# Kernel tuning notes

Measured on AMD Instinct MI355X. Metric: run time of the kernel, lower is better.

## Reference

```python
import jax, jax.numpy as jnp
import numpy as np

G, K, H = 4, 8, 512  # gate_dim, k blocks, block size

def setup_inputs() -> dict:
    key = jax.random.key(0)
    kx, kA, kB = jax.random.split(key, 3)
    x = jax.random.normal(kx, (4096, K * H), dtype=jnp.float32)
    # xavier_normal for (h,h) matrices: std = sqrt(2/(h+h)) = 1/sqrt(h)
    std = 1.0 / np.sqrt(H)
    A = jax.random.normal(kA, (G, H, H), dtype=jnp.float32) * std
    B = jax.random.normal(kB, (G, H, H), dtype=jnp.float32) * std
    return {"x": x, "A": A, "B": B}

def reference(x, A, B):
    # W = blockdiag-style: row block (g,i), col block j -> A_g if i==j else B_g.
    # y[b, g, i, :] = x_i @ A_g^T + (sum_j x_j - x_i) @ B_g^T
    #              = x_i @ (A_g - B_g)^T + S @ B_g^T
    bsz = x.shape[0]
    x3 = x.reshape(bsz, K, H)                      # [B, k, h]
    S = x3.sum(axis=1)                              # [B, h]
    diag_part = jnp.einsum('bkh,gph->bgkp', x3, A - B)   # [B, g, k, h]
    sum_part = jnp.einsum('bh,gph->bgp', S, B)           # [B, g, h]
    out = diag_part + sum_part[:, :, None, :]
    return out.reshape(bsz, G * K * H)
```

## Files before the change

kernel.cpp:

```cpp
#include <hip/hip_runtime.h>

typedef _Float16 f16x8 __attribute__((ext_vector_type(8)));
typedef _Float16 f16x4 __attribute__((ext_vector_type(4)));
typedef _Float16 f16x2 __attribute__((ext_vector_type(2)));
typedef float f32x4 __attribute__((ext_vector_type(4)));
typedef float f32x2 __attribute__((ext_vector_type(2)));

#define GLD_LDS16(gp, lp)                                                        \
  __builtin_amdgcn_global_load_lds(                                              \
      (const __attribute__((address_space(1))) void*)(gp),                       \
      (__attribute__((address_space(3))) void*)(lp), 16, 0, 0)

__global__ void prep_weights_k(const float* __restrict__ A, const float* __restrict__ B,
                               _Float16* __restrict__ Cw, _Float16* __restrict__ Bw) {
  int gid = blockIdx.x * 256 + threadIdx.x;
  f32x4 a = ((const f32x4*)A)[gid];
  f32x4 b = ((const f32x4*)B)[gid];
  f16x4 c, bb;
  c.x = (_Float16)(a.x - b.x); c.y = (_Float16)(a.y - b.y);
  c.z = (_Float16)(a.z - b.z); c.w = (_Float16)(a.w - b.w);
  bb.x = (_Float16)b.x; bb.y = (_Float16)b.y;
  bb.z = (_Float16)b.z; bb.w = (_Float16)b.w;
  ((f16x4*)Cw)[gid] = c;
  ((f16x4*)Bw)[gid] = bb;
}

__global__ void prep_x_k(const float* __restrict__ x, _Float16* __restrict__ xh,
                         _Float16* __restrict__ Sh) {
  int b = blockIdx.x, t = threadIdx.x;
  const f32x2* xr = (const f32x2*)(x + (size_t)b * 4096);
  f16x2* xo = (f16x2*)xh + (size_t)b * 2048;
  float s0 = 0.f, s1 = 0.f;
#pragma unroll
  for (int i = 0; i < 8; ++i) {
    f32x2 v = xr[i * 256 + t];
    f16x2 h;
    h.x = (_Float16)v.x; h.y = (_Float16)v.y;
    xo[i * 256 + t] = h;
    s0 += v.x; s1 += v.y;
  }
  f16x2 sv;
  sv.x = (_Float16)s0; sv.y = (_Float16)s1;
  ((f16x2*)Sh)[(size_t)b * 256 + t] = sv;
}

__global__ __launch_bounds__(256) void gemm_fused_k(const _Float16* __restrict__ Am,
                                                    const _Float16* __restrict__ Cw,
                                                    const _Float16* __restrict__ Bw,
                                                    const _Float16* __restrict__ Sh,
                                                    float* __restrict__ out) {
  __shared__ __align__(16) _Float16 lA[128 * 32];
  __shared__ __align__(16) _Float16 lW[128 * 32];
  __shared__ __align__(16) _Float16 lV[128 * 32];
  __shared__ __align__(16) _Float16 lS[16 * 32];

  const int tid = threadIdx.x;
  const int lane = tid & 63;
  const int wv = tid >> 6;
  const int tile_n = blockIdx.x & 15;
  const int tile_m = blockIdx.x >> 4;

  const _Float16* gA[2];
  const _Float16* gW[2];
  const _Float16* gV[2];
  _Float16* lpA[2];
  _Float16* lpW[2];
  _Float16* lpV[2];
#pragma unroll
  for (int i = 0; i < 2; ++i) {
    int c = i * 256 + tid;
    int row = c >> 2;
    int lc = (c & 3) ^ ((row >> 1) & 3);
    gA[i] = Am + ((size_t)(tile_m * 128 + row) * 512 + lc * 8);
    gW[i] = Cw + ((size_t)(tile_n * 128 + row) * 512 + lc * 8);
    gV[i] = Bw + ((size_t)(tile_n * 128 + row) * 512 + lc * 8);
    lpA[i] = &lA[(i * 256 + wv * 64) * 8];
    lpW[i] = &lW[(i * 256 + wv * 64) * 8];
    lpV[i] = &lV[(i * 256 + wv * 64) * 8];
  }
  const _Float16* gS =
      Sh + ((size_t)(tile_m * 16 + (lane >> 2)) * 512 + (lane & 3) * 8);

  const int lm = lane & 15;
  const int q = lane >> 4;
  const int mw = (wv >> 1) * 64;
  const int nw = (wv & 1) * 64;

  int aoff[4], boff[4], voff[2];
#pragma unroll
  for (int f = 0; f < 4; ++f) {
    int rA = mw + f * 16 + lm;
    aoff[f] = rA * 32 + (q ^ ((rA >> 1) & 3)) * 8;
    int rB = nw + f * 16 + lm;
    boff[f] = rB * 32 + (q ^ ((rB >> 1) & 3)) * 8;
  }
#pragma unroll
  for (int f = 0; f < 2; ++f) {
    int rV = wv * 32 + f * 16 + lm;
    voff[f] = rV * 32 + (q ^ ((rV >> 1) & 3)) * 8;
  }
  const int soff = lm * 32 + q * 8;

  f32x4 acc[4][4];
  f32x4 tacc[2];
#pragma unroll
  for (int im = 0; im < 4; ++im)
#pragma unroll
    for (int in = 0; in < 4; ++in) acc[im][in] = (f32x4){0.f, 0.f, 0.f, 0.f};
#pragma unroll
  for (int f = 0; f < 2; ++f) tacc[f] = (f32x4){0.f, 0.f, 0.f, 0.f};

  for (int kt = 0; kt < 16; ++kt) {
    __syncthreads();
#pragma unroll
    for (int i = 0; i < 2; ++i) {
      GLD_LDS16(gA[i] + kt * 32, lpA[i]);
      GLD_LDS16(gW[i] + kt * 32, lpW[i]);
      GLD_LDS16(gV[i] + kt * 32, lpV[i]);
    }
    if (wv == 0) GLD_LDS16(gS + kt * 32, &lS[0]);
    __syncthreads();
    f16x8 af[4], bf[4], vf[2], sf;
    sf = *(const f16x8*)&lS[soff];
#pragma unroll
    for (int f = 0; f < 4; ++f) {
      af[f] = *(const f16x8*)&lA[aoff[f]];
      bf[f] = *(const f16x8*)&lW[boff[f]];
    }
#pragma unroll
    for (int f = 0; f < 2; ++f) vf[f] = *(const f16x8*)&lV[voff[f]];
#pragma unroll
    for (int im = 0; im < 4; ++im)
#pragma unroll
      for (int in = 0; in < 4; ++in)
        acc[im][in] =
            __builtin_amdgcn_mfma_f32_16x16x32_f16(af[im], bf[in], acc[im][in], 0, 0, 0);
#pragma unroll
    for (int f = 0; f < 2; ++f)
      tacc[f] = __builtin_amdgcn_mfma_f32_16x16x32_f16(sf, vf[f], tacc[f], 0, 0, 0);
  }

  __syncthreads();
  float* lT = (float*)lA;
#pragma unroll
  for (int f = 0; f < 2; ++f) {
    int colb = wv * 32 + f * 16 + lm;
#pragma unroll
    for (int r = 0; r < 4; ++r) lT[(q * 4 + r) * 128 + colb] = tacc[f][r];
  }
  __syncthreads();

#pragma unroll
  for (int im = 0; im < 4; ++im) {
    const int mloc = mw + im * 16 + q * 4;
    const int mbase = tile_m * 128 + mloc;
    const int b = mbase >> 3;
    const int bl = mloc >> 3;
#pragma unroll
    for (int in = 0; in < 4; ++in) {
      const int cl = nw + in * 16 + lm;
      const int col = tile_n * 128 + cl;
      const float tv = lT[bl * 128 + cl];
      f32x4 v = acc[im][in];
      float* op = out + (size_t)b * 16384 + (size_t)(col >> 9) * 4096 +
                  (size_t)(mbase & 7) * 512 + (col & 511);
#pragma unroll
      for (int r = 0; r < 4; ++r) op[r * 512] = v[r] + tv;
    }
  }
}

extern "C" void kernel_launch(void* const* d_in, const int* in_sizes, int n_in,
                              void* d_out, int out_size, void* d_ws, size_t ws_size,
                              hipStream_t stream) {
  const float* x = (const float*)d_in[0];
  const float* A = (const float*)d_in[1];
  const float* B = (const float*)d_in[2];
  float* out = (float*)d_out;
  char* ws = (char*)d_ws;

  _Float16* xh = (_Float16*)(ws);
  _Float16* Sh = (_Float16*)(ws + 33554432u);
  _Float16* Cw = (_Float16*)(ws + 37748736u);
  _Float16* Bw = (_Float16*)(ws + 39845888u);

  prep_weights_k<<<1024, 256, 0, stream>>>(A, B, Cw, Bw);
  prep_x_k<<<4096, 256, 0, stream>>>(x, xh, Sh);
  gemm_fused_k<<<4096, 256, 0, stream>>>(xh, Cw, Bw, Sh, out);
}
```

Before: 420.9 us.

## Double-buffer LDS tiles and prefetch the next K-step during MFMA compute

Converts the single-buffered LDS staging for the x, A-B and B tiles into a two-slot ping-pong buffer. The next K-step's global-to-LDS loads are issued before the current step's MFMAs, and each iteration has one barrier instead of two. The S fragment is now loaded straight from global memory into registers, one step ahead, instead of being staged through LDS. This doubles LDS use per block to about 48 KB, which may lower occupancy, and the compiler's wait on outstanding loads at each barrier may limit how much overlap is achieved.

```diff
diff --git a/kernel.cpp b/kernel.cpp
--- a/kernel.cpp
+++ b/kernel.cpp
@@ -49,10 +49,9 @@
                                                     const _Float16* __restrict__ Bw,
                                                     const _Float16* __restrict__ Sh,
                                                     float* __restrict__ out) {
-  __shared__ __align__(16) _Float16 lA[128 * 32];
-  __shared__ __align__(16) _Float16 lW[128 * 32];
-  __shared__ __align__(16) _Float16 lV[128 * 32];
-  __shared__ __align__(16) _Float16 lS[16 * 32];
+  __shared__ __align__(16) _Float16 lA[2][128 * 32];
+  __shared__ __align__(16) _Float16 lW[2][128 * 32];
+  __shared__ __align__(16) _Float16 lV[2][128 * 32];
 
   const int tid = threadIdx.x;
   const int lane = tid & 63;
@@ -63,9 +62,7 @@
   const _Float16* gA[2];
   const _Float16* gW[2];
   const _Float16* gV[2];
-  _Float16* lpA[2];
-  _Float16* lpW[2];
-  _Float16* lpV[2];
+  int lofs[2];
 #pragma unroll
   for (int i = 0; i < 2; ++i) {
     int c = i * 256 + tid;
@@ -74,12 +71,17 @@
     gA[i] = Am + ((size_t)(tile_m * 128 + row) * 512 + lc * 8);
     gW[i] = Cw + ((size_t)(tile_n * 128 + row) * 512 + lc * 8);
     gV[i] = Bw + ((size_t)(tile_n * 128 + row) * 512 + lc * 8);
-    lpA[i] = &lA[(i * 256 + wv * 64) * 8];
-    lpW[i] = &lW[(i * 256 + wv * 64) * 8];
-    lpV[i] = &lV[(i * 256 + wv * 64) * 8];
+    lofs[i] = (i * 256 + wv * 64) * 8;
   }
-  const _Float16* gS =
-      Sh + ((size_t)(tile_m * 16 + (lane >> 2)) * 512 + (lane & 3) * 8);
+
+#define STAGE_STEP(BUF, KT)                                \
+  do {                                                     \
+    _Pragma("unroll") for (int i = 0; i < 2; ++i) {        \
+      GLD_LDS16(gA[i] + (KT) * 32, &lA[BUF][lofs[i]]);     \
+      GLD_LDS16(gW[i] + (KT) * 32, &lW[BUF][lofs[i]]);     \
+      GLD_LDS16(gV[i] + (KT) * 32, &lV[BUF][lofs[i]]);     \
+    }                                                      \
+  } while (0)
 
   const int lm = lane & 15;
   const int q = lane >> 4;
@@ -99,7 +101,7 @@
     int rV = wv * 32 + f * 16 + lm;
     voff[f] = rV * 32 + (q ^ ((rV >> 1) & 3)) * 8;
   }
-  const int soff = lm * 32 + q * 8;
+  const _Float16* gS = Sh + ((size_t)(tile_m * 16 + lm) * 512 + q * 8);
 
   f32x4 acc[4][4];
   f32x4 tacc[2];
@@ -110,25 +112,26 @@
 #pragma unroll
   for (int f = 0; f < 2; ++f) tacc[f] = (f32x4){0.f, 0.f, 0.f, 0.f};
 
+  f16x8 sfr[2];
+  sfr[0] = *(const f16x8*)gS;
+  STAGE_STEP(0, 0);
+  __syncthreads();
+
+#pragma unroll
   for (int kt = 0; kt < 16; ++kt) {
-    __syncthreads();
-#pragma unroll
-    for (int i = 0; i < 2; ++i) {
-      GLD_LDS16(gA[i] + kt * 32, lpA[i]);
-      GLD_LDS16(gW[i] + kt * 32, lpW[i]);
-      GLD_LDS16(gV[i] + kt * 32, lpV[i]);
+    const int B = kt & 1;
+    if (kt < 15) {
+      sfr[(kt + 1) & 1] = *(const f16x8*)(gS + (kt + 1) * 32);
+      STAGE_STEP((kt + 1) & 1, kt + 1);
     }
-    if (wv == 0) GLD_LDS16(gS + kt * 32, &lS[0]);
-    __syncthreads();
-    f16x8 af[4], bf[4], vf[2], sf;
-    sf = *(const f16x8*)&lS[soff];
+    f16x8 af[4], bf[4], vf[2];
 #pragma unroll
     for (int f = 0; f < 4; ++f) {
-      af[f] = *(const f16x8*)&lA[aoff[f]];
-      bf[f] = *(const f16x8*)&lW[boff[f]];
+      af[f] = *(const f16x8*)&lA[B][aoff[f]];
+      bf[f] = *(const f16x8*)&lW[B][boff[f]];
     }
 #pragma unroll
-    for (int f = 0; f < 2; ++f) vf[f] = *(const f16x8*)&lV[voff[f]];
+    for (int f = 0; f < 2; ++f) vf[f] = *(const f16x8*)&lV[B][voff[f]];
 #pragma unroll
     for (int im = 0; im < 4; ++im)
 #pragma unroll
@@ -137,11 +140,11 @@
             __builtin_amdgcn_mfma_f32_16x16x32_f16(af[im], bf[in], acc[im][in], 0, 0, 0);
 #pragma unroll
     for (int f = 0; f < 2; ++f)
-      tacc[f] = __builtin_amdgcn_mfma_f32_16x16x32_f16(sf, vf[f], tacc[f], 0, 0, 0);
+      tacc[f] = __builtin_amdgcn_mfma_f32_16x16x32_f16(sfr[B], vf[f], tacc[f], 0, 0, 0);
+    __syncthreads();
   }
 
-  __syncthreads();
-  float* lT = (float*)lA;
+  float* lT = (float*)&lA[0][0];
 #pragma unroll
   for (int f = 0; f < 2; ++f) {
     int colb = wv * 32 + f * 16 + lm;
@@ -168,6 +171,7 @@
       for (int r = 0; r < 4; ++r) op[r * 512] = v[r] + tv;
     }
   }
+#undef STAGE_STEP
 }
 
 extern "C" void kernel_launch(void* const* d_in, const int* in_sizes, int n_in,
```

After: 424.7 us. Within noise of the previous version (+0.9%).
